# Kernel tuning notes

Measured on AMD Instinct MI355X. Metric: run time of the kernel, lower is better.

The kernel has to match this reference:

```python
import jax, jax.numpy as jnp
import numpy as np

WS = 7
HEADS = 8
DIM = 256
IN_DIM = 128
HID = 1024
EPS = 1e-5


def _rel_index(ws):
    coords = np.stack(np.meshgrid(np.arange(ws), np.arange(ws), indexing='ij'))  # (2,ws,ws)
    cf = coords.reshape(2, -1)                      # (2,N)
    rel = (cf[:, :, None] - cf[:, None, :]).transpose(1, 2, 0).copy()  # (N,N,2)
    rel[..., 0] += ws - 1
    rel[..., 1] += ws - 1
    rel[..., 0] *= 2 * ws - 1
    return rel.sum(-1)  # (N,N) int

REL_IDX = jnp.asarray(_rel_index(WS).reshape(-1))


def layernorm(x, g, b):
    mu = jnp.mean(x, axis=-1, keepdims=True)
    var = jnp.mean(jnp.square(x - mu), axis=-1, keepdims=True)
    return (x - mu) * jax.lax.rsqrt(var + EPS) * g + b


def setup_inputs() -> dict:
    key = jax.random.key(0)
    ks = jax.random.split(key, 16)
    s = 0.02
    return {
        'x': jax.random.normal(ks[0], (16, IN_DIM, 56, 56), jnp.float32),
        'conv_w': jax.random.normal(ks[1], (DIM, IN_DIM, 3, 3), jnp.float32) * s,
        'conv_b': jnp.zeros((DIM,), jnp.float32),
        'g1': jnp.ones((DIM,), jnp.float32), 'b1': jnp.zeros((DIM,), jnp.float32),
        'g2': jnp.ones((DIM,), jnp.float32), 'b2': jnp.zeros((DIM,), jnp.float32),
        'g3': jnp.ones((DIM,), jnp.float32), 'b3': jnp.zeros((DIM,), jnp.float32),
        'qkv_w': jax.random.normal(ks[2], (3 * DIM, DIM), jnp.float32) * s,
        'rel_bias_table': jax.random.normal(ks[3], ((2 * WS - 1) ** 2, HEADS), jnp.float32) * s,
        'proj_w': jax.random.normal(ks[4], (DIM, DIM), jnp.float32) * s,
        'proj_b': jnp.zeros((DIM,), jnp.float32),
        'fc1_w': jax.random.normal(ks[5], (HID, DIM), jnp.float32) * s,
        'fc1_b': jnp.zeros((HID,), jnp.float32),
        'fc2_w': jax.random.normal(ks[6], (DIM, HID), jnp.float32) * s,
        'fc2_b': jnp.zeros((DIM,), jnp.float32),
    }


def reference(x, conv_w, conv_b, g1, b1, g2, b2, g3, b3, qkv_w, rel_bias_table,
              proj_w, proj_b, fc1_w, fc1_b, fc2_w, fc2_b):
    # proj_q: 3x3 conv, stride 1, pad 1 (input_dim != embed_dim)
    x = jax.lax.conv_general_dilated(
        x, conv_w, window_strides=(1, 1), padding=((1, 1), (1, 1)),
        dimension_numbers=('NCHW', 'OIHW', 'NCHW')) + conv_b[None, :, None, None]
    b, c, h, w = x.shape
    x = x.reshape(b, c, h * w).transpose(0, 2, 1)  # (b, n, c)
    x = layernorm(x, g1, b1)
    x = x.reshape(b, h, w, c)
    pb = (WS - h % WS) % WS
    pr = (WS - w % WS) % WS
    x = jnp.pad(x, ((0, 0), (0, pb), (0, pr), (0, 0)))
    hp, wp = h + pb, w + pr
    # window partition -> (nW, N, c)
    xw = x.reshape(b, hp // WS, WS, wp // WS, WS, c)
    xw = xw.transpose(0, 1, 3, 2, 4, 5).reshape(-1, WS * WS, c)
    nW, N, _ = xw.shape
    d = c // HEADS
    qkv = (xw @ qkv_w.T).reshape(nW, N, 3, HEADS, d).transpose(2, 0, 3, 1, 4)  # (3,nW,h,N,d)
    q, k, v = qkv[0] * (d ** -0.5), qkv[1], qkv[2]
    attn = jnp.einsum('whnd,whmd->whnm', q, k)
    bias = rel_bias_table[REL_IDX].reshape(N, N, HEADS).transpose(2, 0, 1)  # (h,N,N)
    attn = jax.nn.softmax(attn + bias[None], axis=-1)
    out = jnp.einsum('whnm,whmd->whnd', attn, v).transpose(0, 2, 1, 3).reshape(nW, N, c)
    out = out @ proj_w.T + proj_b
    # window reverse
    x = out.reshape(b, hp // WS, wp // WS, WS, WS, c)
    x = x.transpose(0, 1, 3, 2, 4, 5).reshape(b, hp, wp, c)
    x = x[:, :h, :w, :].reshape(b, h * w, c)
    # NOTE: faithful to source — NO residual from pre-attention stream
    x = layernorm(x, g2, b2)
    x = jax.nn.gelu(x @ fc1_w.T + fc1_b, approximate=False) @ fc2_w.T + fc2_b
    x = x + x  # source: x = x + drop_path(x) with identity drop_path
    x = layernorm(x, g3, b3)
    return x.reshape(b, h, w, c).transpose(0, 3, 1, 2)
```

## Files before the change

kernel.cpp:

```cpp
#include <hip/hip_runtime.h>
#include <hip/hip_bf16.h>

typedef unsigned short u16;
typedef unsigned int   u32;

#define TTOK  50176
#define CDIM  256

using short8 = __attribute__((ext_vector_type(8))) short;
using f32x4  = __attribute__((ext_vector_type(4))) float;

__device__ __forceinline__ float b2f(u16 u) { return __uint_as_float(((u32)u) << 16); }
__device__ __forceinline__ u16 f2b(float f) {
    u32 x = __float_as_uint(f);
    return (u16)((x + 0x7fffu + ((x >> 16) & 1u)) >> 16);
}

__global__ __launch_bounds__(256) void cvt_k(const float* __restrict__ in, u16* __restrict__ out, int n4) {
    int i = blockIdx.x * 256 + threadIdx.x;
    if (i >= n4) return;
    float4 v = *(const float4*)&in[i * 4];
    ushort4 o;
    o.x = f2b(v.x); o.y = f2b(v.y); o.z = f2b(v.z); o.w = f2b(v.w);
    *(ushort4*)&out[i * 4] = o;
}

__global__ __launch_bounds__(256) void pad_k(const float* __restrict__ x, u16* __restrict__ xp) {
    __shared__ float tile[128][58];
    int bid = blockIdx.x;
    int b = bid / 58, hp = bid - b * 58;
    int tid = threadIdx.x;
    bool zrow = (hp == 0 || hp == 57);
    if (!zrow) {
        int h = hp - 1;
        for (int e = tid; e < 128 * 14; e += 256) {
            int ic = e / 14, j = e - ic * 14;
            float4 v = *(const float4*)&x[(((size_t)b * 128 + ic) * 56 + h) * 56 + j * 4];
            tile[ic][j * 4 + 0] = v.x; tile[ic][j * 4 + 1] = v.y;
            tile[ic][j * 4 + 2] = v.z; tile[ic][j * 4 + 3] = v.w;
        }
        __syncthreads();
    }
    size_t rb = ((size_t)b * 58 + hp) * 58 * 128;
    for (int u = tid; u < 58 * 16; u += 256) {
        int wp = u / 16, icg = u - wp * 16;
        uint4 o = make_uint4(0u, 0u, 0u, 0u);
        if (!zrow && wp != 0 && wp != 57) {
            int w = wp - 1, ic0 = icg * 8;
            u16 v0 = f2b(tile[ic0 + 0][w]), v1 = f2b(tile[ic0 + 1][w]);
            u16 v2 = f2b(tile[ic0 + 2][w]), v3 = f2b(tile[ic0 + 3][w]);
            u16 v4 = f2b(tile[ic0 + 4][w]), v5 = f2b(tile[ic0 + 5][w]);
            u16 v6 = f2b(tile[ic0 + 6][w]), v7 = f2b(tile[ic0 + 7][w]);
            o.x = (u32)v0 | ((u32)v1 << 16);
            o.y = (u32)v2 | ((u32)v3 << 16);
            o.z = (u32)v4 | ((u32)v5 << 16);
            o.w = (u32)v6 | ((u32)v7 << 16);
        }
        *(uint4*)&xp[rb + (size_t)wp * 128 + icg * 8] = o;
    }
}

__global__ __launch_bounds__(256) void w2_k(const float* __restrict__ w, u16* __restrict__ o2) {
    int e = blockIdx.x * 256 + threadIdx.x;
    int o = e / 1152, rem = e - o * 1152;
    int tap = rem >> 7, ic = rem & 127;
    o2[e] = f2b(w[(o * 128 + ic) * 9 + tap]);
}

__global__ __launch_bounds__(256) void gemm_conv_k(const u16* __restrict__ xp, const u16* __restrict__ W2,
                                                   const float* __restrict__ bias, u16* __restrict__ C) {
    __shared__ __align__(16) u16 lsA[128 * 32];
    __shared__ __align__(16) u16 lsB[128 * 32];
    int tid = threadIdx.x;
    int wave = tid >> 6, lane = tid & 63;
    int mBase = blockIdx.y * 128, nBase = blockIdx.x * 128;
    int wm = wave >> 1, wn = wave & 1;
    int lr = lane & 15, lq = lane >> 4;
    int rowC = lane >> 2, koff = (lane & 3) * 8;
    int c0 = wave * 2, c1 = c0 + 1;

    int t0 = mBase + c0 * 16 + rowC;
    int t1 = mBase + c1 * 16 + rowC;
    size_t tb0, tb1;
    {
        int win = t0 / 49, n = t0 - win * 49;
        int b = win >> 6, wh = (win >> 3) & 7, ww = win & 7;
        int r = n / 7, s = n - r * 7;
        tb0 = ((size_t)(b * 58 + wh * 7 + r) * 58 + ww * 7 + s) * 128 + koff;
    }
    {
        int win = t1 / 49, n = t1 - win * 49;
        int b = win >> 6, wh = (win >> 3) & 7, ww = win & 7;
        int r = n / 7, s = n - r * 7;
        tb1 = ((size_t)(b * 58 + wh * 7 + r) * 58 + ww * 7 + s) * 128 + koff;
    }
    const u16* gB0 = W2 + (size_t)(nBase + c0 * 16 + rowC) * 1152 + koff;
    const u16* gB1 = W2 + (size_t)(nBase + c1 * 16 + rowC) * 1152 + koff;

    f32x4 acc[4][4];
#pragma unroll
    for (int m = 0; m < 4; ++m)
#pragma unroll
        for (int n = 0; n < 4; ++n) acc[m][n] = (f32x4){0.f, 0.f, 0.f, 0.f};

    for (int ks = 0; ks < 36; ++ks) {
        int tap = ks >> 2, ic0 = (ks & 3) * 32;
        int kh = tap / 3, kw = tap - kh * 3;
        int uoff = (kh * 58 + kw) * 128 + ic0;
        int k0 = ks * 32;
        __builtin_amdgcn_global_load_lds((const __attribute__((address_space(1))) void*)(xp + tb0 + uoff),
                                         (__attribute__((address_space(3))) void*)(lsA + c0 * 512), 16, 0, 0);
        __builtin_amdgcn_global_load_lds((const __attribute__((address_space(1))) void*)(xp + tb1 + uoff),
                                         (__attribute__((address_space(3))) void*)(lsA + c1 * 512), 16, 0, 0);
        __builtin_amdgcn_global_load_lds((const __attribute__((address_space(1))) void*)(gB0 + k0),
                                         (__attribute__((address_space(3))) void*)(lsB + c0 * 512), 16, 0, 0);
        __builtin_amdgcn_global_load_lds((const __attribute__((address_space(1))) void*)(gB1 + k0),
                                         (__attribute__((address_space(3))) void*)(lsB + c1 * 512), 16, 0, 0);
        __syncthreads();
        short8 af[4], bf[4];
#pragma unroll
        for (int m = 0; m < 4; ++m)
            af[m] = *(const short8*)&lsA[(wm * 64 + m * 16 + lr) * 32 + lq * 8];
#pragma unroll
        for (int n = 0; n < 4; ++n)
            bf[n] = *(const short8*)&lsB[(wn * 64 + n * 16 + lr) * 32 + lq * 8];
#pragma unroll
        for (int m = 0; m < 4; ++m)
#pragma unroll
            for (int n = 0; n < 4; ++n)
                acc[m][n] = __builtin_amdgcn_mfma_f32_16x16x32_bf16(af[m], bf[n], acc[m][n], 0, 0, 0);
        __syncthreads();
    }

#pragma unroll
    for (int m = 0; m < 4; ++m) {
        int row0 = mBase + wm * 64 + m * 16 + lq * 4;
#pragma unroll
        for (int n = 0; n < 4; ++n) {
            int col = nBase + wn * 64 + n * 16 + lr;
            float bv = bias[col];
#pragma unroll
            for (int r = 0; r < 4; ++r)
                C[(size_t)(row0 + r) * 256 + col] = f2b(acc[m][n][r] + bv);
        }
    }
}

template <int EPI>
__global__ __launch_bounds__(256) void gemm_k(const u16* __restrict__ A, const u16* __restrict__ Bw,
                                              const float* __restrict__ bias, u16* __restrict__ C,
                                              int M, int N, int K) {
    __shared__ __align__(16) u16 lsA[128 * 32];
    __shared__ __align__(16) u16 lsB[128 * 32];
    int tid = threadIdx.x;
    int wave = tid >> 6, lane = tid & 63;
    int mBase = blockIdx.y * 128, nBase = blockIdx.x * 128;
    int wm = wave >> 1, wn = wave & 1;
    int lr = lane & 15, lq = lane >> 4;

    int rowC = lane >> 2;
    int koff = (lane & 3) * 8;
    int c0 = wave * 2, c1 = wave * 2 + 1;
    const u16* gA0 = A + (size_t)(mBase + c0 * 16 + rowC) * K + koff;
    const u16* gA1 = A + (size_t)(mBase + c1 * 16 + rowC) * K + koff;
    const u16* gB0 = Bw + (size_t)(nBase + c0 * 16 + rowC) * K + koff;
    const u16* gB1 = Bw + (size_t)(nBase + c1 * 16 + rowC) * K + koff;

    f32x4 acc[4][4];
#pragma unroll
    for (int m = 0; m < 4; ++m)
#pragma unroll
        for (int n = 0; n < 4; ++n) acc[m][n] = (f32x4){0.f, 0.f, 0.f, 0.f};

    for (int k0 = 0; k0 < K; k0 += 32) {
        __builtin_amdgcn_global_load_lds((const __attribute__((address_space(1))) void*)(gA0 + k0),
                                         (__attribute__((address_space(3))) void*)(lsA + c0 * 512), 16, 0, 0);
        __builtin_amdgcn_global_load_lds((const __attribute__((address_space(1))) void*)(gA1 + k0),
                                         (__attribute__((address_space(3))) void*)(lsA + c1 * 512), 16, 0, 0);
        __builtin_amdgcn_global_load_lds((const __attribute__((address_space(1))) void*)(gB0 + k0),
                                         (__attribute__((address_space(3))) void*)(lsB + c0 * 512), 16, 0, 0);
        __builtin_amdgcn_global_load_lds((const __attribute__((address_space(1))) void*)(gB1 + k0),
                                         (__attribute__((address_space(3))) void*)(lsB + c1 * 512), 16, 0, 0);
        __syncthreads();
        short8 af[4], bf[4];
#pragma unroll
        for (int m = 0; m < 4; ++m)
            af[m] = *(const short8*)&lsA[(wm * 64 + m * 16 + lr) * 32 + lq * 8];
#pragma unroll
        for (int n = 0; n < 4; ++n)
            bf[n] = *(const short8*)&lsB[(wn * 64 + n * 16 + lr) * 32 + lq * 8];
#pragma unroll
        for (int m = 0; m < 4; ++m)
#pragma unroll
            for (int n = 0; n < 4; ++n)
                acc[m][n] = __builtin_amdgcn_mfma_f32_16x16x32_bf16(af[m], bf[n], acc[m][n], 0, 0, 0);
        __syncthreads();
    }

#pragma unroll
    for (int m = 0; m < 4; ++m) {
        int row0 = mBase + wm * 64 + m * 16 + lq * 4;
#pragma unroll
        for (int n = 0; n < 4; ++n) {
            int col = nBase + wn * 64 + n * 16 + lr;
            float bv = (EPI >= 1) ? bias[col] : 0.f;
#pragma unroll
            for (int r = 0; r < 4; ++r) {
                float v = acc[m][n][r] + bv;
                if (EPI == 2) v = 0.5f * v * (1.f + erff(v * 0.70710678118654752f));
                C[(size_t)(row0 + r) * N + col] = f2b(v);
            }
        }
    }
}

__global__ __launch_bounds__(256) void ln_k(u16* __restrict__ y, const float* __restrict__ g,
                                            const float* __restrict__ bta) {
    int wid = (blockIdx.x << 2) + (threadIdx.x >> 6);
    int lane = threadIdx.x & 63;
    u16* row = y + (size_t)wid * CDIM;
    ushort4 u = *(const ushort4*)&row[lane * 4];
    float v0 = b2f(u.x), v1 = b2f(u.y), v2 = b2f(u.z), v3 = b2f(u.w);
    float s = v0 + v1 + v2 + v3;
    float q = v0 * v0 + v1 * v1 + v2 * v2 + v3 * v3;
#pragma unroll
    for (int o = 32; o; o >>= 1) { s += __shfl_xor(s, o); q += __shfl_xor(q, o); }
    float mean = s * (1.f / 256.f);
    float var = q * (1.f / 256.f) - mean * mean;
    float inv = rsqrtf(var + 1e-5f);
    float4 gg = *(const float4*)&g[lane * 4];
    float4 bb = *(const float4*)&bta[lane * 4];
    ushort4 o4;
    o4.x = f2b((v0 - mean) * inv * gg.x + bb.x);
    o4.y = f2b((v1 - mean) * inv * gg.y + bb.y);
    o4.z = f2b((v2 - mean) * inv * gg.z + bb.z);
    o4.w = f2b((v3 - mean) * inv * gg.w + bb.w);
    *(ushort4*)&row[lane * 4] = o4;
}

__global__ __launch_bounds__(256) void attn_mfma_k(const u16* __restrict__ qkv,
                                                   const float* __restrict__ tab,
                                                   u16* __restrict__ out) {
    __shared__ __align__(16) u16 sh[28488];
    int tid = threadIdx.x;
    int wave = tid >> 6, lane = tid & 63;
    int wh = blockIdx.x * 4 + wave;
    int win = wh >> 3, head = wh & 7;
    int g = lane >> 4, cc = lane & 15;

    u16* Pl = sh + wave * 4608;
    u16* Vl = sh + 18432 + wave * 2176;
    float* bs = (float*)(sh + 27136) + wave * 169;

    const size_t wbase = (size_t)win * 49 * 768;
    for (int e = lane; e < 169; e += 64) bs[e] = tab[e * 8 + head];
    for (int e = lane; e < 49 * 16; e += 64) {
        int k = e >> 4, d0 = (e & 15) * 2;
        *(u32*)&Vl[k * 34 + d0] = *(const u32*)&qkv[wbase + (size_t)k * 768 + 512 + head * 32 + d0];
    }
    for (int e = lane; e < 15 * 16; e += 64) {
        int k = 49 + (e >> 4), d0 = (e & 15) * 2;
        *(u32*)&Vl[k * 34 + d0] = 0u;
    }
    __syncthreads();

    short8 aQ[4], bK[4];
#pragma unroll
    for (int t = 0; t < 4; ++t) {
        int qr = t * 16 + cc; if (qr > 48) qr = 48;
        aQ[t] = *(const short8*)&qkv[wbase + (size_t)qr * 768 + head * 32 + g * 8];
        int kr = t * 16 + cc; if (kr > 48) kr = 48;
        bK[t] = *(const short8*)&qkv[wbase + (size_t)kr * 768 + 256 + head * 32 + g * 8];
    }
    f32x4 S[4][4];
#pragma unroll
    for (int a = 0; a < 4; ++a)
#pragma unroll
        for (int b = 0; b < 4; ++b)
            S[a][b] = __builtin_amdgcn_mfma_f32_16x16x32_bf16(aQ[a], bK[b], (f32x4){0.f,0.f,0.f,0.f}, 0, 0, 0);

    int AqA[4][4];
#pragma unroll
    for (int tr = 0; tr < 4; ++tr)
#pragma unroll
        for (int r = 0; r < 4; ++r) {
            int q = tr * 16 + g * 4 + r; if (q > 48) q = 48;
            int dq = (q * 37) >> 8;
            AqA[tr][r] = 6 * dq + q + 84;
        }
    int AcA[4];
    bool colBad[4];
#pragma unroll
    for (int tc = 0; tc < 4; ++tc) {
        int c = tc * 16 + cc;
        colBad[tc] = (c > 48);
        if (c > 48) c = 48;
        int dc = (c * 37) >> 8;
        AcA[tc] = 6 * dc + c;
    }
    const float scale = 0.17677669529663687f;
    float inv[4][4];
#pragma unroll
    for (int tr = 0; tr < 4; ++tr) {
#pragma unroll
        for (int r = 0; r < 4; ++r) {
            float z0 = colBad[0] ? -1e30f : S[tr][0][r] * scale + bs[AqA[tr][r] - AcA[0]];
            float z1 = colBad[1] ? -1e30f : S[tr][1][r] * scale + bs[AqA[tr][r] - AcA[1]];
            float z2 = colBad[2] ? -1e30f : S[tr][2][r] * scale + bs[AqA[tr][r] - AcA[2]];
            float z3 = colBad[3] ? -1e30f : S[tr][3][r] * scale + bs[AqA[tr][r] - AcA[3]];
            float mx = fmaxf(fmaxf(z0, z1), fmaxf(z2, z3));
            mx = fmaxf(mx, __shfl_xor(mx, 1));
            mx = fmaxf(mx, __shfl_xor(mx, 2));
            mx = fmaxf(mx, __shfl_xor(mx, 4));
            mx = fmaxf(mx, __shfl_xor(mx, 8));
            float p0 = __expf(z0 - mx), p1 = __expf(z1 - mx);
            float p2 = __expf(z2 - mx), p3 = __expf(z3 - mx);
            S[tr][0][r] = p0; S[tr][1][r] = p1; S[tr][2][r] = p2; S[tr][3][r] = p3;
            float sm = p0 + p1 + p2 + p3;
            sm += __shfl_xor(sm, 1); sm += __shfl_xor(sm, 2);
            sm += __shfl_xor(sm, 4); sm += __shfl_xor(sm, 8);
            inv[tr][r] = 1.0f / sm;
        }
    }

#pragma unroll
    for (int tr = 0; tr < 4; ++tr)
#pragma unroll
        for (int tc = 0; tc < 4; ++tc) {
            int k = tc * 16 + cc;
            u16* pb = &Pl[tr * 1152 + k * 18 + g * 4];
            u32 w0 = (u32)f2b(S[tr][tc][0]) | ((u32)f2b(S[tr][tc][1]) << 16);
            u32 w1 = (u32)f2b(S[tr][tc][2]) | ((u32)f2b(S[tr][tc][3]) << 16);
            *(u32*)pb = w0;
            *(u32*)(pb + 2) = w1;
        }
    __syncthreads();

    f32x4 O[4][2];
#pragma unroll
    for (int a = 0; a < 4; ++a) { O[a][0] = (f32x4){0.f,0.f,0.f,0.f}; O[a][1] = (f32x4){0.f,0.f,0.f,0.f}; }
#pragma unroll
    for (int s = 0; s < 2; ++s) {
        short8 pa[4], vb[2];
#pragma unroll
        for (int tr = 0; tr < 4; ++tr)
#pragma unroll
            for (int j = 0; j < 8; ++j)
                pa[tr][j] = (short)Pl[tr * 1152 + (s * 32 + g * 8 + j) * 18 + cc];
#pragma unroll
        for (int td = 0; td < 2; ++td)
#pragma unroll
            for (int j = 0; j < 8; ++j)
                vb[td][j] = (short)Vl[(s * 32 + g * 8 + j) * 34 + td * 16 + cc];
#pragma unroll
        for (int tr = 0; tr < 4; ++tr)
#pragma unroll
            for (int td = 0; td < 2; ++td)
                O[tr][td] = __builtin_amdgcn_mfma_f32_16x16x32_bf16(pa[tr], vb[td], O[tr][td], 0, 0, 0);
    }

#pragma unroll
    for (int tr = 0; tr < 4; ++tr)
#pragma unroll
        for (int r = 0; r < 4; ++r) {
            int q = tr * 16 + g * 4 + r;
            if (q < 49) {
                float iv = inv[tr][r];
                u16* op = out + (size_t)(win * 49 + q) * 256 + head * 32;
                op[cc]      = f2b(O[tr][0][r] * iv);
                op[16 + cc] = f2b(O[tr][1][r] * iv);
            }
        }
}

__global__ __launch_bounds__(256) void ln3_out_k(const u16* __restrict__ f, const float* __restrict__ g3,
                                                 const float* __restrict__ b3, float* __restrict__ out) {
    __shared__ float tile[256][57];
    int bh = blockIdx.x;
    int b = bh / 56, h = bh - b * 56;
    int wv = threadIdx.x >> 6, lane = threadIdx.x & 63;
    int wh = h / 7, r = h - wh * 7;
    float4 gg = *(const float4*)&g3[lane * 4];
    float4 bb = *(const float4*)&b3[lane * 4];
    for (int i = 0; i < 14; ++i) {
        int w = wv + i * 4;
        int wwn = w / 7, s2 = w - wwn * 7;
        int t = (b * 64 + wh * 8 + wwn) * 49 + r * 7 + s2;
        ushort4 u = *(const ushort4*)&f[(size_t)t * 256 + lane * 4];
        float v0 = 2.f * b2f(u.x), v1 = 2.f * b2f(u.y), v2 = 2.f * b2f(u.z), v3 = 2.f * b2f(u.w);
        float s = v0 + v1 + v2 + v3;
        float q = v0 * v0 + v1 * v1 + v2 * v2 + v3 * v3;
#pragma unroll
        for (int o = 32; o; o >>= 1) { s += __shfl_xor(s, o); q += __shfl_xor(q, o); }
        float mean = s * (1.f / 256.f);
        float var = q * (1.f / 256.f) - mean * mean;
        float inv = rsqrtf(var + 1e-5f);
        int c = lane * 4;
        tile[c + 0][w] = (v0 - mean) * inv * gg.x + bb.x;
        tile[c + 1][w] = (v1 - mean) * inv * gg.y + bb.y;
        tile[c + 2][w] = (v2 - mean) * inv * gg.z + bb.z;
        tile[c + 3][w] = (v3 - mean) * inv * gg.w + bb.w;
    }
    __syncthreads();
    size_t obase = (size_t)b * 256 * 3136 + (size_t)h * 56;
#pragma unroll
    for (int it = 0; it < 28; ++it) {
        int e = it * 256 + threadIdx.x;
        int c = e / 28, wu = e - c * 28;
        float2 pack = make_float2(tile[c][wu * 2], tile[c][wu * 2 + 1]);
        *(float2*)&out[obase + (size_t)c * 3136 + wu * 2] = pack;
    }
}

extern "C" void kernel_launch(void* const* d_in, const int* in_sizes, int n_in,
                              void* d_out, int out_size, void* d_ws, size_t ws_size,
                              hipStream_t stream) {
    (void)in_sizes; (void)n_in; (void)out_size;
    const float* x      = (const float*)d_in[0];
    const float* conv_w = (const float*)d_in[1];
    const float* conv_b = (const float*)d_in[2];
    const float* g1     = (const float*)d_in[3];
    const float* b1     = (const float*)d_in[4];
    const float* g2     = (const float*)d_in[5];
    const float* b2     = (const float*)d_in[6];
    const float* g3     = (const float*)d_in[7];
    const float* b3     = (const float*)d_in[8];
    const float* qkv_w  = (const float*)d_in[9];
    const float* tab    = (const float*)d_in[10];
    const float* proj_w = (const float*)d_in[11];
    const float* proj_b = (const float*)d_in[12];
    const float* fc1_w  = (const float*)d_in[13];
    const float* fc1_b  = (const float*)d_in[14];
    const float* fc2_w  = (const float*)d_in[15];
    const float* fc2_b  = (const float*)d_in[16];
    float* outp = (float*)d_out;

    const size_t OFF_Y  = (size_t)TTOK * 1152 * 2;
    const size_t OFF_AT = OFF_Y + (size_t)TTOK * 512;
    const size_t NEED   = OFF_AT + (size_t)TTOK * 512;
    if (ws_size < NEED) return;

    char* ws = (char*)d_ws;
    u16* xpad    = (u16*)ws;
    u16* ybuf    = (u16*)(ws + OFF_Y);
    u16* atout   = (u16*)(ws + OFF_AT);
    u16* qkvbuf  = (u16*)ws;
    u16* hidden  = (u16*)ws;
    u16* W2      = atout;
    u16* wbase   = (u16*)(ws + (size_t)TTOK * 1024 * 2);
    u16* qkvw_b  = wbase;
    u16* projw_b = wbase + 196608;
    u16* fc1w_b  = projw_b + 65536;
    u16* fc2w_b  = fc1w_b + 262144;

    pad_k<<<928, 256, 0, stream>>>(x, xpad);
    w2_k<<<1152, 256, 0, stream>>>(conv_w, W2);
    cvt_k<<<192, 256, 0, stream>>>(qkv_w, qkvw_b, 49152);
    cvt_k<<<64,  256, 0, stream>>>(proj_w, projw_b, 16384);
    cvt_k<<<256, 256, 0, stream>>>(fc1_w, fc1w_b, 65536);
    cvt_k<<<256, 256, 0, stream>>>(fc2_w, fc2w_b, 65536);
    gemm_conv_k<<<dim3(2, 392), 256, 0, stream>>>(xpad, W2, conv_b, ybuf);
    ln_k<<<12544, 256, 0, stream>>>(ybuf, g1, b1);
    gemm_k<0><<<dim3(6, 392), 256, 0, stream>>>(ybuf, qkvw_b, nullptr, qkvbuf, TTOK, 768, 256);
    attn_mfma_k<<<2048, 256, 0, stream>>>(qkvbuf, tab, atout);
    gemm_k<1><<<dim3(2, 392), 256, 0, stream>>>(atout, projw_b, proj_b, ybuf, TTOK, 256, 256);
    ln_k<<<12544, 256, 0, stream>>>(ybuf, g2, b2);
    gemm_k<2><<<dim3(8, 392), 256, 0, stream>>>(ybuf, fc1w_b, fc1_b, hidden, TTOK, 1024, 256);
    gemm_k<1><<<dim3(2, 392), 256, 0, stream>>>(hidden, fc2w_b, fc2_b, atout, TTOK, 256, 1024);
    ln3_out_k<<<896, 256, 0, stream>>>(atout, g3, b3, outp);
}
```

Before: 382.1 us.

## Double K-tile to 64 with XOR-swizzled LDS and XCD-aware block remap in GEMMs

Both the conv GEMM and the generic GEMM now stage 64-wide K slices per barrier pair instead of 32, halving the number of sync rounds. Global-to-LDS loads are reorganized into 8-row chunks, with an XOR swizzle on the 16-byte column group to avoid LDS bank conflicts on fragment reads. A block remap groups consecutive M tiles on the same XCD to improve L2 reuse. LDS use per block doubles, which may lower occupancy.

Result: faster. 332.6 us (-13.0%).

```diff
diff --git a/kernel.cpp b/kernel.cpp
--- a/kernel.cpp
+++ b/kernel.cpp
@@ -15,6 +15,10 @@
     u32 x = __float_as_uint(f);
     return (u16)((x + 0x7fffu + ((x >> 16) & 1u)) >> 16);
 }
+
+#define GLD16(src, dst) __builtin_amdgcn_global_load_lds( \
+    (const __attribute__((address_space(1))) void*)(src),  \
+    (__attribute__((address_space(3))) void*)(dst), 16, 0, 0)
 
 __global__ __launch_bounds__(256) void cvt_k(const float* __restrict__ in, u16* __restrict__ out, int n4) {
     int i = blockIdx.x * 256 + threadIdx.x;
@@ -67,35 +71,39 @@
     o2[e] = f2b(w[(o * 128 + ic) * 9 + tap]);
 }
 
+__device__ __forceinline__ void xcd_remap(int& bx, int& by) {
+    int nx = gridDim.x, ny = gridDim.y;
+    if ((ny & 7) == 0) {
+        int linear = blockIdx.y * nx + blockIdx.x;
+        int xcd = linear & 7, within = linear >> 3;
+        bx = within % nx;
+        by = xcd * (ny >> 3) + within / nx;
+    } else { bx = blockIdx.x; by = blockIdx.y; }
+}
+
 __global__ __launch_bounds__(256) void gemm_conv_k(const u16* __restrict__ xp, const u16* __restrict__ W2,
                                                    const float* __restrict__ bias, u16* __restrict__ C) {
-    __shared__ __align__(16) u16 lsA[128 * 32];
-    __shared__ __align__(16) u16 lsB[128 * 32];
+    __shared__ __align__(16) u16 lsA[128 * 64];
+    __shared__ __align__(16) u16 lsB[128 * 64];
     int tid = threadIdx.x;
     int wave = tid >> 6, lane = tid & 63;
-    int mBase = blockIdx.y * 128, nBase = blockIdx.x * 128;
+    int bx, by; xcd_remap(bx, by);
+    int mBase = by * 128, nBase = bx * 128;
     int wm = wave >> 1, wn = wave & 1;
     int lr = lane & 15, lq = lane >> 4;
-    int rowC = lane >> 2, koff = (lane & 3) * 8;
-    int c0 = wave * 2, c1 = c0 + 1;
-
-    int t0 = mBase + c0 * 16 + rowC;
-    int t1 = mBase + c1 * 16 + rowC;
-    size_t tb0, tb1;
-    {
-        int win = t0 / 49, n = t0 - win * 49;
+    int r8 = lane >> 3, kg = lane & 7;
+    int kgsw = ((kg ^ r8) & 7) * 8;
+
+    size_t tb[4]; const u16* gB[4];
+#pragma unroll
+    for (int i = 0; i < 4; ++i) {
+        int t = mBase + (wave * 4 + i) * 8 + r8;
+        int win = t / 49, n = t - win * 49;
         int b = win >> 6, wh = (win >> 3) & 7, ww = win & 7;
         int r = n / 7, s = n - r * 7;
-        tb0 = ((size_t)(b * 58 + wh * 7 + r) * 58 + ww * 7 + s) * 128 + koff;
-    }
-    {
-        int win = t1 / 49, n = t1 - win * 49;
-        int b = win >> 6, wh = (win >> 3) & 7, ww = win & 7;
-        int r = n / 7, s = n - r * 7;
-        tb1 = ((size_t)(b * 58 + wh * 7 + r) * 58 + ww * 7 + s) * 128 + koff;
-    }
-    const u16* gB0 = W2 + (size_t)(nBase + c0 * 16 + rowC) * 1152 + koff;
-    const u16* gB1 = W2 + (size_t)(nBase + c1 * 16 + rowC) * 1152 + koff;
+        tb[i] = ((size_t)(b * 58 + wh * 7 + r) * 58 + ww * 7 + s) * 128 + kgsw;
+        gB[i] = W2 + (size_t)(nBase + (wave * 4 + i) * 8 + r8) * 1152 + kgsw;
+    }
 
     f32x4 acc[4][4];
 #pragma unroll
@@ -103,32 +111,33 @@
 #pragma unroll
         for (int n = 0; n < 4; ++n) acc[m][n] = (f32x4){0.f, 0.f, 0.f, 0.f};
 
-    for (int ks = 0; ks < 36; ++ks) {
-        int tap = ks >> 2, ic0 = (ks & 3) * 32;
+    for (int ks = 0; ks < 18; ++ks) {
+        int tap = ks >> 1, half = ks & 1;
         int kh = tap / 3, kw = tap - kh * 3;
-        int uoff = (kh * 58 + kw) * 128 + ic0;
-        int k0 = ks * 32;
-        __builtin_amdgcn_global_load_lds((const __attribute__((address_space(1))) void*)(xp + tb0 + uoff),
-                                         (__attribute__((address_space(3))) void*)(lsA + c0 * 512), 16, 0, 0);
-        __builtin_amdgcn_global_load_lds((const __attribute__((address_space(1))) void*)(xp + tb1 + uoff),
-                                         (__attribute__((address_space(3))) void*)(lsA + c1 * 512), 16, 0, 0);
-        __builtin_amdgcn_global_load_lds((const __attribute__((address_space(1))) void*)(gB0 + k0),
-                                         (__attribute__((address_space(3))) void*)(lsB + c0 * 512), 16, 0, 0);
-        __builtin_amdgcn_global_load_lds((const __attribute__((address_space(1))) void*)(gB1 + k0),
-                                         (__attribute__((address_space(3))) void*)(lsB + c1 * 512), 16, 0, 0);
+        int uoff = (kh * 58 + kw) * 128 + half * 64;
+#pragma unroll
+        for (int i = 0; i < 4; ++i) {
+            int crow = wave * 4 + i;
+            GLD16(xp + tb[i] + uoff, lsA + crow * 512);
+            GLD16(gB[i] + ks * 64,   lsB + crow * 512);
+        }
         __syncthreads();
-        short8 af[4], bf[4];
-#pragma unroll
-        for (int m = 0; m < 4; ++m)
-            af[m] = *(const short8*)&lsA[(wm * 64 + m * 16 + lr) * 32 + lq * 8];
-#pragma unroll
-        for (int n = 0; n < 4; ++n)
-            bf[n] = *(const short8*)&lsB[(wn * 64 + n * 16 + lr) * 32 + lq * 8];
-#pragma unroll
-        for (int m = 0; m < 4; ++m)
+#pragma unroll
+        for (int kk = 0; kk < 2; ++kk) {
+            int sl = (((kk << 2) | lq) ^ (lr & 7)) * 8;
+            short8 af[4], bf[4];
+#pragma unroll
+            for (int m = 0; m < 4; ++m)
+                af[m] = *(const short8*)&lsA[(wm * 64 + m * 16 + lr) * 64 + sl];
 #pragma unroll
             for (int n = 0; n < 4; ++n)
-                acc[m][n] = __builtin_amdgcn_mfma_f32_16x16x32_bf16(af[m], bf[n], acc[m][n], 0, 0, 0);
+                bf[n] = *(const short8*)&lsB[(wn * 64 + n * 16 + lr) * 64 + sl];
+#pragma unroll
+            for (int m = 0; m < 4; ++m)
+#pragma unroll
+                for (int n = 0; n < 4; ++n)
+                    acc[m][n] = __builtin_amdgcn_mfma_f32_16x16x32_bf16(af[m], bf[n], acc[m][n], 0, 0, 0);
+        }
         __syncthreads();
     }
 
@@ -150,21 +159,24 @@
 __global__ __launch_bounds__(256) void gemm_k(const u16* __restrict__ A, const u16* __restrict__ Bw,
                                               const float* __restrict__ bias, u16* __restrict__ C,
                                               int M, int N, int K) {
-    __shared__ __align__(16) u16 lsA[128 * 32];
-    __shared__ __align__(16) u16 lsB[128 * 32];
+    __shared__ __align__(16) u16 lsA[128 * 64];
+    __shared__ __align__(16) u16 lsB[128 * 64];
     int tid = threadIdx.x;
     int wave = tid >> 6, lane = tid & 63;
-    int mBase = blockIdx.y * 128, nBase = blockIdx.x * 128;
+    int bx, by; xcd_remap(bx, by);
+    int mBase = by * 128, nBase = bx * 128;
     int wm = wave >> 1, wn = wave & 1;
     int lr = lane & 15, lq = lane >> 4;
-
-    int rowC = lane >> 2;
-    int koff = (lane & 3) * 8;
-    int c0 = wave * 2, c1 = wave * 2 + 1;
-    const u16* gA0 = A + (size_t)(mBase + c0 * 16 + rowC) * K + koff;
-    const u16* gA1 = A + (size_t)(mBase + c1 * 16 + rowC) * K + koff;
-    const u16* gB0 = Bw + (size_t)(nBase + c0 * 16 + rowC) * K + koff;
-    const u16* gB1 = Bw + (size_t)(nBase + c1 * 16 + rowC) * K + koff;
+    int r8 = lane >> 3, kg = lane & 7;
+    int kgsw = ((kg ^ r8) & 7) * 8;
+
+    const u16* gA[4]; const u16* gB[4];
+#pragma unroll
+    for (int i = 0; i < 4; ++i) {
+        int crow = wave * 4 + i;
+        gA[i] = A  + (size_t)(mBase + crow * 8 + r8) * K + kgsw;
+        gB[i] = Bw + (size_t)(nBase + crow * 8 + r8) * K + kgsw;
+    }
 
     f32x4 acc[4][4];
 #pragma unroll
@@ -172,28 +184,30 @@
 #pragma unroll
         for (int n = 0; n < 4; ++n) acc[m][n] = (f32x4){0.f, 0.f, 0.f, 0.f};
 
-    for (int k0 = 0; k0 < K; k0 += 32) {
-        __builtin_amdgcn_global_load_lds((const __attribute__((address_space(1))) void*)(gA0 + k0),
-                                         (__attribute__((address_space(3))) void*)(lsA + c0 * 512), 16, 0, 0);
-        __builtin_amdgcn_global_load_lds((const __attribute__((address_space(1))) void*)(gA1 + k0),
-                                         (__attribute__((address_space(3))) void*)(lsA + c1 * 512), 16, 0, 0);
-        __builtin_amdgcn_global_load_lds((const __attribute__((address_space(1))) void*)(gB0 + k0),
-                                         (__attribute__((address_space(3))) void*)(lsB + c0 * 512), 16, 0, 0);
-        __builtin_amdgcn_global_load_lds((const __attribute__((address_space(1))) void*)(gB1 + k0),
-                                         (__attribute__((address_space(3))) void*)(lsB + c1 * 512), 16, 0, 0);
+    for (int k0 = 0; k0 < K; k0 += 64) {
+#pragma unroll
+        for (int i = 0; i < 4; ++i) {
+            int crow = wave * 4 + i;
+            GLD16(gA[i] + k0, lsA + crow * 512);
+            GLD16(gB[i] + k0, lsB + crow * 512);
+        }
         __syncthreads();
-        short8 af[4], bf[4];
-#pragma unroll
-        for (int m = 0; m < 4; ++m)
-            af[m] = *(const short8*)&lsA[(wm * 64 + m * 16 + lr) * 32 + lq * 8];
-#pragma unroll
-        for (int n = 0; n < 4; ++n)
-            bf[n] = *(const short8*)&lsB[(wn * 64 + n * 16 + lr) * 32 + lq * 8];
-#pragma unroll
-        for (int m = 0; m < 4; ++m)
+#pragma unroll
+        for (int kk = 0; kk < 2; ++kk) {
+            int sl = (((kk << 2) | lq) ^ (lr & 7)) * 8;
+            short8 af[4], bf[4];
+#pragma unroll
+            for (int m = 0; m < 4; ++m)
+                af[m] = *(const short8*)&lsA[(wm * 64 + m * 16 + lr) * 64 + sl];
 #pragma unroll
             for (int n = 0; n < 4; ++n)
-                acc[m][n] = __builtin_amdgcn_mfma_f32_16x16x32_bf16(af[m], bf[n], acc[m][n], 0, 0, 0);
+                bf[n] = *(const short8*)&lsB[(wn * 64 + n * 16 + lr) * 64 + sl];
+#pragma unroll
+            for (int m = 0; m < 4; ++m)
+#pragma unroll
+                for (int n = 0; n < 4; ++n)
+                    acc[m][n] = __builtin_amdgcn_mfma_f32_16x16x32_bf16(af[m], bf[n], acc[m][n], 0, 0, 0);
+        }
         __syncthreads();
     }
 
```
